# Optimization experiments

Measured on AMD Instinct MI355X. Metric: run time of the kernel, lower is better.

## Reference

```python
import jax, jax.numpy as jnp
import numpy as np

NC = 128      # nc
K = 5         # cube kernel size
NS = 3        # n_scale pyramid levels
NV = 150000   # vertices (cortical-surface scale)
NF = 300000   # faces ~ 2*NV
L = 192       # volume side (L = W = H -> rescale = [1,1,1])


def setup_inputs() -> dict:
    key = jax.random.key(0)
    ks = jax.random.split(key, 16)
    s = 0.05
    return {
        "v": jax.random.uniform(ks[0], (1, NV, 3), minval=-0.9, maxval=0.9, dtype=jnp.float32),
        "f": jax.random.randint(ks[1], (1, NF, 3), 0, NV, dtype=jnp.int32),
        "volume": jax.random.normal(ks[2], (1, 1, L, L, L), dtype=jnp.float32),
        "fc1_w": jax.random.normal(ks[3], (6, NC), dtype=jnp.float32) * s,
        "fc1_b": jnp.zeros((NC,), jnp.float32),
        "fc2_w": jax.random.normal(ks[4], (2 * NC, 4 * NC), dtype=jnp.float32) * s,
        "fc2_b": jnp.zeros((4 * NC,), jnp.float32),
        "fc3_w": jax.random.normal(ks[5], (4 * NC, 2 * NC), dtype=jnp.float32) * s,
        "fc3_b": jnp.zeros((2 * NC,), jnp.float32),
        "fc4_w": jax.random.normal(ks[6], (2 * NC, 3), dtype=jnp.float32) * s,
        "fc4_b": jnp.zeros((3,), jnp.float32),
        "conv_w": jax.random.normal(ks[7], (NC, NS, K, K, K), dtype=jnp.float32) * s,
        "conv_b": jnp.zeros((NC,), jnp.float32),
        "lfc_w": jax.random.normal(ks[8], (NC, NC), dtype=jnp.float32) * s,
        "lfc_b": jnp.zeros((NC,), jnp.float32),
    }


def _vertex_normals(v, f):
    # pytorch3d-style vertex normals: scatter-add area-weighted face normals, then normalize.
    verts, faces = v[0], f[0]
    p0, p1, p2 = verts[faces[:, 0]], verts[faces[:, 1]], verts[faces[:, 2]]
    fn = jnp.cross(p1 - p0, p2 - p0)  # [NF, 3]
    n = jnp.zeros_like(verts)
    n = n.at[faces[:, 0]].add(fn).at[faces[:, 1]].add(fn).at[faces[:, 2]].add(fn)
    n = n / jnp.maximum(jnp.linalg.norm(n, axis=-1, keepdims=True), 1e-12)
    return n[None]  # [1, NV, 3]


def _cube_sampling(v, volume):
    # Vectorized version of the 125-iteration Python gather loop:
    # gather a KxKxK neighborhood per vertex at each pyramid scale.
    vol_n = volume[0, 0]
    off = jnp.arange(-(K - 1) // 2, (K - 1) // 2 + 1)  # [-2..2]
    cubes = []
    for n in range(NS):
        if n > 0:
            s = vol_n.shape[0]
            vol_n = vol_n.reshape(s // 2, 2, s // 2, 2, s // 2, 2).mean(axis=(1, 3, 5))  # avg_pool3d(2)
        idx = jnp.round((v[0] + 1.0) * L / 2 ** (n + 1)).astype(jnp.int32)  # rescale = [1,1,1]
        idx = jnp.clip(idx, (K - 1) // 2, L // 2 ** n - 3)
        i0 = idx[:, 0, None, None, None] + off[None, :, None, None]
        i1 = idx[:, 1, None, None, None] + off[None, None, :, None]
        i2 = idx[:, 2, None, None, None] + off[None, None, None, :]
        cubes.append(vol_n[i0, i1, i2])  # [NV, K, K, K]
    return jnp.stack(cubes, axis=1)  # [NV, NS, K, K, K]


def reference(v, f, volume, fc1_w, fc1_b, fc2_w, fc2_b, fc3_w, fc3_b, fc4_w, fc4_b,
              conv_w, conv_b, lfc_w, lfc_b):
    coord = v
    normal = _vertex_normals(v, f)
    x = jnp.concatenate([v, normal], axis=2)                 # [1, NV, 6]
    x = jax.nn.leaky_relu(x @ fc1_w + fc1_b, 0.15)           # [1, NV, NC]
    cubes = _cube_sampling(v, volume)                        # [NV, NS, K, K, K]
    # Conv3d with kernel == input size -> single output voxel == full contraction.
    x_local = jnp.einsum('ncijk,ocijk->no', cubes, conv_w) + conv_b  # [NV, NC]
    x_local = (x_local @ lfc_w + lfc_b)[None]                # [1, NV, NC]
    x = jnp.concatenate([x, x_local], axis=2)                # [1, NV, 2*NC]
    x = jax.nn.leaky_relu(x @ fc2_w + fc2_b, 0.15)
    x = jax.nn.leaky_relu(x @ fc3_w + fc3_b, 0.15)
    x = jnp.tanh(x @ fc4_w + fc4_b) * 0.1
    return coord + x
```

## Files before the change

### kernel.cpp

```cpp
#include <hip/hip_runtime.h>
#include <hip/hip_bf16.h>
#include <math.h>

#define NVERT 150000
#define NFACE 300000
#define LVOL  192
#define TVB   32
#define MTV   48

#define NB_NORM   1172
#define NB_POOL1  3456
#define NB_POOL2  432
#define NB_PW     1024
#define NB_PC     193
#define NB_CP0    3456
#define POOL1_START (NB_NORM)
#define POOL2_START (NB_NORM + NB_POOL1)
#define PW_START    (NB_NORM + NB_POOL1 + NB_POOL2)
#define PC_START    (NB_NORM + NB_POOL1 + NB_POOL2 + NB_PW)
#define NB_MEGA     (NB_NORM + NB_POOL1 + NB_POOL2 + NB_PW + NB_PC)

#define WS_BIG_NEED 44808576ull
#define WS_B16_NEED 58964352ull

typedef short v8s __attribute__((ext_vector_type(8)));
typedef float v4f __attribute__((ext_vector_type(4)));

__device__ __forceinline__ float s2f(short s) {
    unsigned int u = ((unsigned int)(unsigned short)s) << 16;
    return __builtin_bit_cast(float, u);
}
__device__ __forceinline__ short f2s(float f) {
    __hip_bfloat16 h = __float2bfloat16(f);
    return __builtin_bit_cast(short, h);
}
__device__ __forceinline__ float lrelu(float x) { return x > 0.f ? x : 0.15f * x; }

__device__ __forceinline__ float ldf(const void* __restrict__ p, int i, int bf) {
    return bf ? s2f(((const short*)p)[i]) : ((const float*)p)[i];
}

__device__ __forceinline__ int haddr(int r, int c) {
    int hi  = c >> 7;
    int mid = (c >> 4) & 7;
    int lo  = c & 15;
    int wc  = hi * 64 + (mid & 3) * 16 + lo;
    return ((mid < 4) ? 0 : 12672) + r * 264 + wc;
}

__global__ void detect_kernel(const void* __restrict__ v, int* __restrict__ flag) {
    __shared__ int s_ok;
    int t = threadIdx.x;
    if (t == 0) s_ok = 1;
    __syncthreads();
    float x = s2f(((const short*)v)[t]);
    if (!(fabsf(x) <= 1.0f)) atomicAnd(&s_ok, 0);
    __syncthreads();
    if (t == 0) *flag = s_ok;
}

__global__ __launch_bounds__(256) void mega_prep_kernel(
    const void* __restrict__ v, const int* __restrict__ f, float* __restrict__ n_accum,
    const void* __restrict__ volume,
    short* __restrict__ vol1b, short* __restrict__ vol2b,
    const void* __restrict__ fc2_w, const void* __restrict__ fc3_w,
    short* __restrict__ fc2T, short* __restrict__ fc3T,
    const void* __restrict__ conv_w, const void* __restrict__ lfc_w,
    const void* __restrict__ conv_b, const void* __restrict__ lfc_b,
    short* __restrict__ Wcomb, float* __restrict__ bcomb,
    const int* __restrict__ flag,
    short* __restrict__ vol0b)
{
    const int bf = *flag;
    const int bid = blockIdx.x;
    const int t = threadIdx.x;

    if (bid < NB_NORM) {
        int ft = bid * 256 + t;
        if (ft >= NFACE) return;
        int i0 = f[ft * 3 + 0], i1 = f[ft * 3 + 1], i2 = f[ft * 3 + 2];
        float p0x = ldf(v, i0 * 3 + 0, bf), p0y = ldf(v, i0 * 3 + 1, bf), p0z = ldf(v, i0 * 3 + 2, bf);
        float p1x = ldf(v, i1 * 3 + 0, bf), p1y = ldf(v, i1 * 3 + 1, bf), p1z = ldf(v, i1 * 3 + 2, bf);
        float p2x = ldf(v, i2 * 3 + 0, bf), p2y = ldf(v, i2 * 3 + 1, bf), p2z = ldf(v, i2 * 3 + 2, bf);
        float e1x = p1x - p0x, e1y = p1y - p0y, e1z = p1z - p0z;
        float e2x = p2x - p0x, e2y = p2y - p0y, e2z = p2z - p0z;
        float cx = e1y * e2z - e1z * e2y;
        float cy = e1z * e2x - e1x * e2z;
        float cz = e1x * e2y - e1y * e2x;
        atomicAdd(&n_accum[i0 * 3 + 0], cx); atomicAdd(&n_accum[i0 * 3 + 1], cy); atomicAdd(&n_accum[i0 * 3 + 2], cz);
        atomicAdd(&n_accum[i1 * 3 + 0], cx); atomicAdd(&n_accum[i1 * 3 + 1], cy); atomicAdd(&n_accum[i1 * 3 + 2], cz);
        atomicAdd(&n_accum[i2 * 3 + 0], cx); atomicAdd(&n_accum[i2 * 3 + 1], cy); atomicAdd(&n_accum[i2 * 3 + 2], cz);
    } else if (bid < POOL2_START) {
        int id = (bid - POOL1_START) * 256 + t;
        int z = id % 96, y = (id / 96) % 96, x = id / (96 * 96);
        float s = 0.f;
        #pragma unroll
        for (int a = 0; a < 2; a++)
            #pragma unroll
            for (int b = 0; b < 2; b++)
                #pragma unroll
                for (int c = 0; c < 2; c++)
                    s += ldf(volume, (2 * x + a) * (LVOL * LVOL) + (2 * y + b) * LVOL + (2 * z + c), bf);
        s *= 0.125f;
        vol1b[id] = f2s(s);
    } else if (bid < PW_START) {
        int id = (bid - POOL2_START) * 256 + t;
        int z = id % 48, y = (id / 48) % 48, x = id / (48 * 48);
        float s = 0.f;
        for (int a = 0; a < 4; a++)
            for (int b = 0; b < 4; b++)
                #pragma unroll
                for (int c = 0; c < 4; c++)
                    s += ldf(volume, (4 * x + a) * (LVOL * LVOL) + (4 * y + b) * LVOL + (4 * z + c), bf);
        s *= 0.015625f;
        vol2b[id] = f2s(s);
    } else if (bid < PC_START) {
        int id = (bid - PW_START) * 256 + t;
        if (id < 131072) {
            int col = id >> 8, k = id & 255;
            int tile = col >> 4, ln = col & 15;
            int kk = k >> 5, r = k & 31, qq = r >> 3, e = r & 7;
            fc2T[((tile * 8 + kk) * 64 + qq * 16 + ln) * 8 + e] = f2s(ldf(fc2_w, k * 512 + col, bf));
        } else {
            int i = id - 131072;
            int col = i >> 9, k = i & 511;
            int tile = col >> 4, ln = col & 15;
            int kk = k >> 5, r = k & 31, qq = r >> 3, e = r & 7;
            fc3T[((tile * 16 + kk) * 64 + qq * 16 + ln) * 8 + e] = f2s(ldf(fc3_w, k * 256 + col, bf));
        }
    } else if (bid < NB_MEGA) {
        int id = (bid - PC_START) * 256 + t;
        if (id < 49152) {
            int j = id / 384, k = id - j * 384;
            float acc = 0.f;
            if (k < 375) {
                float a0 = 0.f, a1 = 0.f, a2 = 0.f, a3 = 0.f;
                for (int o = 0; o < 128; o += 4) {
                    a0 += ldf(conv_w, (o + 0) * 375 + k, bf) * ldf(lfc_w, (o + 0) * 128 + j, bf);
                    a1 += ldf(conv_w, (o + 1) * 375 + k, bf) * ldf(lfc_w, (o + 1) * 128 + j, bf);
                    a2 += ldf(conv_w, (o + 2) * 375 + k, bf) * ldf(lfc_w, (o + 2) * 128 + j, bf);
                    a3 += ldf(conv_w, (o + 3) * 375 + k, bf) * ldf(lfc_w, (o + 3) * 128 + j, bf);
                }
                acc = (a0 + a1) + (a2 + a3);
            }
            int tile = j >> 4, ln = j & 15;
            int kk = k >> 5, r = k & 31, qq = r >> 3, e = r & 7;
            Wcomb[((tile * 12 + kk) * 64 + qq * 16 + ln) * 8 + e] = f2s(acc);
        } else if (id < 49152 + 128) {
            int j = id - 49152;
            float acc = ldf(lfc_b, j, bf);
            for (int o = 0; o < 128; o++) acc += ldf(conv_b, o, bf) * ldf(lfc_w, o * 128 + j, bf);
            bcomb[j] = acc;
        }
    } else {
        if (bf) return;
        int id = (bid - NB_MEGA) * 2048 + t * 8;
        const float* vp = (const float*)volume;
        short tmp[8];
        #pragma unroll
        for (int i = 0; i < 8; i++) tmp[i] = f2s(vp[id + i]);
        *(v8s*)&vol0b[id] = *(v8s*)tmp;
    }
}


__global__ __launch_bounds__(256, 6) void gather_conv_kernel(
    const void* __restrict__ v,
    const void* __restrict__ volume,
    const short* __restrict__ vol1b,
    const short* __restrict__ vol2b,
    const short* __restrict__ vol0b,
    const short* __restrict__ Wcomb,
    const float* __restrict__ bcomb,
    short* __restrict__ xloc,
    const int* __restrict__ flag)
{
    __shared__ __align__(16) short sCube[TVB * 392];
    __shared__ int sIdx[TVB * 4];

    const int bf = *flag;
    const int t = threadIdx.x;
    const int base = blockIdx.x * TVB;
    const int w = t >> 6, L = t & 63, q = L >> 4, ln = L & 15;
    const short* v0 = bf ? (const short*)volume : vol0b;

    if (t < TVB) {
        int vert = min(base + t, NVERT - 1);
        float vx = ldf(v, vert * 3 + 0, bf);
        float vy = ldf(v, vert * 3 + 1, bf);
        float vz = ldf(v, vert * 3 + 2, bf);
        #pragma unroll
        for (int n = 0; n < 3; n++) {
            float scl = (n == 0) ? 96.0f : (n == 1 ? 48.0f : 24.0f);
            int dim = LVOL >> n, lim = dim - 3;
            int cx = min(max((int)rintf((vx + 1.0f) * scl), 2), lim);
            int cy = min(max((int)rintf((vy + 1.0f) * scl), 2), lim);
            int cz = min(max((int)rintf((vz + 1.0f) * scl), 2), lim);
            sIdx[t * 4 + n] = (cx * dim + cy) * dim + (cz - 2);
        }
    }
    __syncthreads();

    for (int idx = t; idx < TVB * 75; idx += 256) {
        int n   = idx / 800;
        int rem = idx - n * 800;
        int vl  = rem / 25;
        int dd  = rem - vl * 25;
        int di  = dd / 5, dj = dd - di * 5;
        int dim = LVOL >> n;
        int addr = sIdx[vl * 4 + n] + (di - 2) * dim * dim + (dj - 2) * dim;
        short* dst = &sCube[vl * 392 + n * 125 + dd * 5];
        if (n == 0 && v0 == nullptr) {
            const float* vp = (const float*)volume;
            #pragma unroll
            for (int i = 0; i < 5; i++) dst[i] = f2s(vp[addr + i]);
        } else {
            const short* lvl = (n == 0) ? v0 : (n == 1 ? vol1b : vol2b);
            #pragma unroll
            for (int i = 0; i < 5; i++) dst[i] = lvl[addr + i];
        }
    }
    for (int idx = t; idx < TVB * 9; idx += 256) {
        int vl = idx / 9, rr = idx - vl * 9;
        sCube[vl * 392 + 375 + rr] = 0;
    }
    __syncthreads();

    #pragma unroll
    for (int nt = 0; nt < 2; nt++) {
        int col = w * 32 + nt * 16 + ln;
        const short* wb = Wcomb + ((w * 2 + nt) * 12 * 64 + q * 16 + ln) * 8;
        v4f acc0 = {0.f, 0.f, 0.f, 0.f}, acc1 = {0.f, 0.f, 0.f, 0.f};
        #pragma unroll
        for (int k0 = 0; k0 < 12; k0++) {
            v8s b  = *(const v8s*)(wb + k0 * 512);
            v8s a0 = *(const v8s*)&sCube[ln * 392 + k0 * 32 + q * 8];
            v8s a1 = *(const v8s*)&sCube[(16 + ln) * 392 + k0 * 32 + q * 8];
            acc0 = __builtin_amdgcn_mfma_f32_16x16x32_bf16(a0, b, acc0, 0, 0, 0);
            acc1 = __builtin_amdgcn_mfma_f32_16x16x32_bf16(a1, b, acc1, 0, 0, 0);
        }
        float bias = bcomb[col];
        #pragma unroll
        for (int r = 0; r < 4; r++) {
            xloc[(base + q * 4 + r) * 128 + col]      = f2s(acc0[r] + bias);
            xloc[(base + 16 + q * 4 + r) * 128 + col] = f2s(acc1[r] + bias);
        }
    }
}

__global__ __launch_bounds__(256, 3) void mlp_kernel(
    const void* __restrict__ v,
    const float* __restrict__ n_accum,
    const short* __restrict__ xloc,
    const short* __restrict__ fc2T,
    const short* __restrict__ fc3T,
    const void* __restrict__ fc1_w, const void* __restrict__ fc1_b,
    const void* __restrict__ fc2_b, const void* __restrict__ fc3_b,
    const void* __restrict__ fc4_w, const void* __restrict__ fc4_b,
    void* __restrict__ out,
    const int* __restrict__ flag)
{
    __shared__ __align__(16) char smem[52224];
    short* sX  = (short*)smem;
    short* sHB = (short*)smem;
    short* s3  = (short*)smem;
    short* sW4 = (short*)(smem + 50688);

    const int bf = *flag;
    const int t = threadIdx.x;
    const int base = blockIdx.x * MTV;
    const int w = t >> 6, L = t & 63, q = L >> 4, ln = L & 15;
    const int laneoff = (q * 16 + ln) * 8;

    for (int id = t; id < MTV * 16; id += 256) {
        int row = id >> 4, seg = id & 15;
        v8s x = *(const v8s*)(xloc + (base + row) * 128 + seg * 8);
        *(v8s*)&sX[row * 264 + 128 + seg * 8] = x;
    }

    for (int i = t; i < 768; i += 256) {
        int j = i >> 8, k = i & 255;
        sW4[i] = f2s(ldf(fc4_w, k * 3 + j, bf));
    }

    {
        int vi = t >> 2, cb = (t & 3) * 32;
        if (vi < MTV) {
            int vert = base + vi;
            float i0 = ldf(v, vert * 3 + 0, bf);
            float i1 = ldf(v, vert * 3 + 1, bf);
            float i2 = ldf(v, vert * 3 + 2, bf);
            float nx = n_accum[vert * 3 + 0];
            float ny = n_accum[vert * 3 + 1];
            float nz = n_accum[vert * 3 + 2];
            float inv = 1.0f / fmaxf(sqrtf(nx * nx + ny * ny + nz * nz), 1e-12f);
            float i3 = nx * inv, i4 = ny * inv, i5 = nz * inv;
            #pragma unroll 8
            for (int i = 0; i < 32; i++) {
                int c = cb + i;
                float acc = ldf(fc1_b, c, bf)
                          + i0 * ldf(fc1_w, 0 * 128 + c, bf)
                          + i1 * ldf(fc1_w, 1 * 128 + c, bf)
                          + i2 * ldf(fc1_w, 2 * 128 + c, bf)
                          + i3 * ldf(fc1_w, 3 * 128 + c, bf)
                          + i4 * ldf(fc1_w, 4 * 128 + c, bf)
                          + i5 * ldf(fc1_w, 5 * 128 + c, bf);
                sX[vi * 264 + c] = f2s(lrelu(acc));
            }
        }
    }
    __syncthreads();

    {
        #pragma unroll
        for (int nt = 4; nt < 8; nt++) {
            int col = w * 128 + nt * 16 + ln;
            const short* bb = fc2T + (w * 8 + nt) * 8 * 512 + laneoff;
            v4f acc0 = {0.f, 0.f, 0.f, 0.f}, acc1 = {0.f, 0.f, 0.f, 0.f}, acc2 = {0.f, 0.f, 0.f, 0.f};
            #pragma unroll
            for (int k0 = 0; k0 < 8; k0++) {
                v8s b  = *(const v8s*)(bb + k0 * 512);
                v8s a0 = *(const v8s*)&sX[(ln) * 264 + k0 * 32 + q * 8];
                v8s a1 = *(const v8s*)&sX[(16 + ln) * 264 + k0 * 32 + q * 8];
                v8s a2 = *(const v8s*)&sX[(32 + ln) * 264 + k0 * 32 + q * 8];
                acc0 = __builtin_amdgcn_mfma_f32_16x16x32_bf16(a0, b, acc0, 0, 0, 0);
                acc1 = __builtin_amdgcn_mfma_f32_16x16x32_bf16(a1, b, acc1, 0, 0, 0);
                acc2 = __builtin_amdgcn_mfma_f32_16x16x32_bf16(a2, b, acc2, 0, 0, 0);
            }
            float bias = ldf(fc2_b, col, bf);
            int wc = 12672 + w * 64 + (nt - 4) * 16 + ln;
            #pragma unroll
            for (int r = 0; r < 4; r++) {
                sHB[(q * 4 + r) * 264 + wc]      = f2s(lrelu(acc0[r] + bias));
                sHB[(16 + q * 4 + r) * 264 + wc] = f2s(lrelu(acc1[r] + bias));
                sHB[(32 + q * 4 + r) * 264 + wc] = f2s(lrelu(acc2[r] + bias));
            }
        }

        v4f accL[4][3];
        #pragma unroll
        for (int nt = 0; nt < 4; nt++)
            #pragma unroll
            for (int m = 0; m < 3; m++)
                accL[nt][m] = (v4f){0.f, 0.f, 0.f, 0.f};

        #pragma unroll
        for (int nt = 0; nt < 4; nt++) {
            const short* bb = fc2T + (w * 8 + nt) * 8 * 512 + laneoff;
            #pragma unroll
            for (int k0 = 0; k0 < 8; k0++) {
                v8s b  = *(const v8s*)(bb + k0 * 512);
                v8s a0 = *(const v8s*)&sX[(ln) * 264 + k0 * 32 + q * 8];
                v8s a1 = *(const v8s*)&sX[(16 + ln) * 264 + k0 * 32 + q * 8];
                v8s a2 = *(const v8s*)&sX[(32 + ln) * 264 + k0 * 32 + q * 8];
                accL[nt][0] = __builtin_amdgcn_mfma_f32_16x16x32_bf16(a0, b, accL[nt][0], 0, 0, 0);
                accL[nt][1] = __builtin_amdgcn_mfma_f32_16x16x32_bf16(a1, b, accL[nt][1], 0, 0, 0);
                accL[nt][2] = __builtin_amdgcn_mfma_f32_16x16x32_bf16(a2, b, accL[nt][2], 0, 0, 0);
            }
        }
        __syncthreads();

        #pragma unroll
        for (int nt = 0; nt < 4; nt++) {
            int col = w * 128 + nt * 16 + ln;
            float bias = ldf(fc2_b, col, bf);
            int wc = w * 64 + nt * 16 + ln;
            #pragma unroll
            for (int r = 0; r < 4; r++) {
                sHB[(q * 4 + r) * 264 + wc]      = f2s(lrelu(accL[nt][0][r] + bias));
                sHB[(16 + q * 4 + r) * 264 + wc] = f2s(lrelu(accL[nt][1][r] + bias));
                sHB[(32 + q * 4 + r) * 264 + wc] = f2s(lrelu(accL[nt][2][r] + bias));
            }
        }
    }
    __syncthreads();

    {
        v4f acc[4][3];
        #pragma unroll
        for (int nt = 0; nt < 4; nt++)
            #pragma unroll
            for (int m = 0; m < 3; m++)
                acc[nt][m] = (v4f){0.f, 0.f, 0.f, 0.f};

        #pragma unroll
        for (int half = 0; half < 2; half++) {
            v8s A0[8], A1[8], A2[8];
            #pragma unroll
            for (int k0 = 0; k0 < 8; k0++) {
                int c = half * 256 + k0 * 32 + q * 8;
                A0[k0] = *(const v8s*)&sHB[haddr(ln, c)];
                A1[k0] = *(const v8s*)&sHB[haddr(16 + ln, c)];
                A2[k0] = *(const v8s*)&sHB[haddr(32 + ln, c)];
            }
            #pragma unroll
            for (int nt = 0; nt < 4; nt++) {
                const short* bb = fc3T + ((w * 4 + nt) * 16 + half * 8) * 512 + laneoff;
                v8s B[8];
                #pragma unroll
                for (int k0 = 0; k0 < 8; k0++) B[k0] = *(const v8s*)(bb + k0 * 512);
                #pragma unroll
                for (int k0 = 0; k0 < 8; k0++) {
                    acc[nt][0] = __builtin_amdgcn_mfma_f32_16x16x32_bf16(A0[k0], B[k0], acc[nt][0], 0, 0, 0);
                    acc[nt][1] = __builtin_amdgcn_mfma_f32_16x16x32_bf16(A1[k0], B[k0], acc[nt][1], 0, 0, 0);
                    acc[nt][2] = __builtin_amdgcn_mfma_f32_16x16x32_bf16(A2[k0], B[k0], acc[nt][2], 0, 0, 0);
                }
            }
        }
        __syncthreads();

        #pragma unroll
        for (int nt = 0; nt < 4; nt++) {
            int col = w * 64 + nt * 16 + ln;
            float bias = ldf(fc3_b, col, bf);
            #pragma unroll
            for (int r = 0; r < 4; r++) {
                s3[(q * 4 + r) * 264 + col]      = f2s(lrelu(acc[nt][0][r] + bias));
                s3[(16 + q * 4 + r) * 264 + col] = f2s(lrelu(acc[nt][1][r] + bias));
                s3[(32 + q * 4 + r) * 264 + col] = f2s(lrelu(acc[nt][2][r] + bias));
            }
        }
    }
    __syncthreads();

    {
        int vi = t >> 2, l = t & 3;
        if (vi < MTV) {
            float p0 = 0.f, p1 = 0.f, p2 = 0.f;
            for (int k = l * 8; k < 256; k += 32) {
                #pragma unroll
                for (int j = 0; j < 8; j++) {
                    float a = s2f(s3[vi * 264 + k + j]);
                    p0 += a * s2f(sW4[0 * 256 + k + j]);
                    p1 += a * s2f(sW4[1 * 256 + k + j]);
                    p2 += a * s2f(sW4[2 * 256 + k + j]);
                }
            }
            #pragma unroll
            for (int s = 2; s; s >>= 1) {
                p0 += __shfl_down(p0, s, 4);
                p1 += __shfl_down(p1, s, 4);
                p2 += __shfl_down(p2, s, 4);
            }
            if (l == 0) {
                int vert = base + vi;
                float vx = ldf(v, vert * 3 + 0, bf);
                float vy = ldf(v, vert * 3 + 1, bf);
                float vz = ldf(v, vert * 3 + 2, bf);
                float o0 = vx + 0.1f * tanhf(p0 + ldf(fc4_b, 0, bf));
                float o1 = vy + 0.1f * tanhf(p1 + ldf(fc4_b, 1, bf));
                float o2 = vz + 0.1f * tanhf(p2 + ldf(fc4_b, 2, bf));
                if (bf) {
                    short* ob = (short*)out;
                    ob[vert * 3 + 0] = f2s(o0);
                    ob[vert * 3 + 1] = f2s(o1);
                    ob[vert * 3 + 2] = f2s(o2);
                } else {
                    float* of = (float*)out;
                    of[vert * 3 + 0] = o0;
                    of[vert * 3 + 1] = o1;
                    of[vert * 3 + 2] = o2;
                }
            }
        }
    }
}

__global__ __launch_bounds__(256, 3) void fused_mfma_kernel(
    const void* __restrict__ v,
    const float* __restrict__ n_accum,
    const void* __restrict__ volume,
    const short* __restrict__ vol1,
    const short* __restrict__ vol2,
    const short* __restrict__ Wcomb,
    const float* __restrict__ bcomb,
    const short* __restrict__ fc2T,
    const short* __restrict__ fc3T,
    const void* __restrict__ fc1_w, const void* __restrict__ fc1_b,
    const void* __restrict__ fc2_b, const void* __restrict__ fc3_b,
    const void* __restrict__ fc4_w, const void* __restrict__ fc4_b,
    void* __restrict__ out,
    const int* __restrict__ flag)
{
    __shared__ __align__(16) char smem[51712];
    short* sX    = (short*)smem;
    short* sCube = (short*)(smem + 16896);
    short* sH    = (short*)(smem + 16896);
    short* s3    = (short*)smem;
    short* sW4   = (short*)(smem + 50176);

    const int bf = *flag;
    const int t = threadIdx.x;
    const int base = blockIdx.x * TVB;
    const int w = t >> 6, L = t & 63, q = L >> 4, ln = L & 15;
    const int laneoff = (q * 16 + ln) * 8;

    for (int idx = t; idx < TVB * 75; idx += 256) {
        int vl  = idx / 75;
        int r75 = idx - vl * 75;
        int n   = r75 / 25;
        int dd  = r75 - n * 25;
        int di  = dd / 5, dj = dd - di * 5;
        int vert = base + vl;
        short* dst = &sCube[vl * 392 + n * 125 + dd * 5];
        if (vert < NVERT) {
            float vx = ldf(v, vert * 3 + 0, bf);
            float vy = ldf(v, vert * 3 + 1, bf);
            float vz = ldf(v, vert * 3 + 2, bf);
            float scl = (n == 0) ? 96.0f : (n == 1 ? 48.0f : 24.0f);
            int lim = (LVOL >> n) - 3;
            int cx = (int)rintf((vx + 1.0f) * scl);
            int cy = (int)rintf((vy + 1.0f) * scl);
            int cz = (int)rintf((vz + 1.0f) * scl);
            cx = min(max(cx, 2), lim) + di - 2;
            cy = min(max(cy, 2), lim) + dj - 2;
            cz = min(max(cz, 2), lim);
            if (n == 0) {
                int b0 = (cx * LVOL + cy) * LVOL + (cz - 2);
                if (bf) {
                    const short* vp = (const short*)volume;
                    #pragma unroll
                    for (int i = 0; i < 5; i++) dst[i] = vp[b0 + i];
                } else {
                    const float* vp = (const float*)volume;
                    #pragma unroll
                    for (int i = 0; i < 5; i++) dst[i] = f2s(vp[b0 + i]);
                }
            } else {
                const short* lvl = (n == 1) ? vol1 : vol2;
                int dim = (n == 1) ? 96 : 48;
                int b0 = (cx * dim + cy) * dim + (cz - 2);
                #pragma unroll
                for (int i = 0; i < 5; i++) dst[i] = lvl[b0 + i];
            }
        } else {
            #pragma unroll
            for (int i = 0; i < 5; i++) dst[i] = 0;
        }
    }
    for (int idx = t; idx < TVB * 9; idx += 256) {
        int vl = idx / 9, rr = idx - vl * 9;
        sCube[vl * 392 + 375 + rr] = 0;
    }
    for (int i = t; i < 768; i += 256) {
        int j = i >> 8, k = i & 255;
        sW4[i] = f2s(ldf(fc4_w, k * 3 + j, bf));
    }
    {
        int vi = t & 31, cb = (t >> 5) * 16;
        int vert = base + vi;
        float i0 = 0.f, i1 = 0.f, i2 = 0.f, i3 = 0.f, i4 = 0.f, i5 = 0.f;
        if (vert < NVERT) {
            i0 = ldf(v, vert * 3 + 0, bf);
            i1 = ldf(v, vert * 3 + 1, bf);
            i2 = ldf(v, vert * 3 + 2, bf);
            float nx = n_accum[vert * 3 + 0];
            float ny = n_accum[vert * 3 + 1];
            float nz = n_accum[vert * 3 + 2];
            float inv = 1.0f / fmaxf(sqrtf(nx * nx + ny * ny + nz * nz), 1e-12f);
            i3 = nx * inv; i4 = ny * inv; i5 = nz * inv;
        }
        #pragma unroll
        for (int i = 0; i < 16; i++) {
            int c = cb + i;
            float acc = ldf(fc1_b, c, bf)
                      + i0 * ldf(fc1_w, 0 * 128 + c, bf)
                      + i1 * ldf(fc1_w, 1 * 128 + c, bf)
                      + i2 * ldf(fc1_w, 2 * 128 + c, bf)
                      + i3 * ldf(fc1_w, 3 * 128 + c, bf)
                      + i4 * ldf(fc1_w, 4 * 128 + c, bf)
                      + i5 * ldf(fc1_w, 5 * 128 + c, bf);
            sX[vi * 264 + c] = f2s(lrelu(acc));
        }
    }
    __syncthreads();

    #pragma unroll
    for (int nt = 0; nt < 2; nt++) {
        int col = w * 32 + nt * 16 + ln;
        const short* wb = Wcomb + ((w * 2 + nt) * 12 * 64) * 8 + laneoff;
        v4f acc0 = {0.f, 0.f, 0.f, 0.f}, acc1 = {0.f, 0.f, 0.f, 0.f};
        #pragma unroll
        for (int k0 = 0; k0 < 12; k0++) {
            v8s b  = *(const v8s*)(wb + k0 * 512);
            v8s a0 = *(const v8s*)&sCube[ln * 392 + k0 * 32 + q * 8];
            v8s a1 = *(const v8s*)&sCube[(16 + ln) * 392 + k0 * 32 + q * 8];
            acc0 = __builtin_amdgcn_mfma_f32_16x16x32_bf16(a0, b, acc0, 0, 0, 0);
            acc1 = __builtin_amdgcn_mfma_f32_16x16x32_bf16(a1, b, acc1, 0, 0, 0);
        }
        float bias = bcomb[col];
        #pragma unroll
        for (int r = 0; r < 4; r++) {
            sX[(q * 4 + r) * 264 + 128 + col]      = f2s(acc0[r] + bias);
            sX[(16 + q * 4 + r) * 264 + 128 + col] = f2s(acc1[r] + bias);
        }
    }
    __syncthreads();

    {
        v8s a0[8], a1[8];
        #pragma unroll
        for (int k0 = 0; k0 < 8; k0++) {
            a0[k0] = *(const v8s*)&sX[ln * 264 + k0 * 32 + q * 8];
            a1[k0] = *(const v8s*)&sX[(16 + ln) * 264 + k0 * 32 + q * 8];
        }
        #pragma unroll
        for (int nt = 0; nt < 8; nt++) {
            int col = w * 128 + nt * 16 + ln;
            const short* bb = fc2T + (w * 8 + nt) * 8 * 512 + laneoff;
            v4f acc0 = {0.f, 0.f, 0.f, 0.f}, acc1 = {0.f, 0.f, 0.f, 0.f};
            #pragma unroll
            for (int k0 = 0; k0 < 8; k0++) {
                v8s b = *(const v8s*)(bb + k0 * 512);
                acc0 = __builtin_amdgcn_mfma_f32_16x16x32_bf16(a0[k0], b, acc0, 0, 0, 0);
                acc1 = __builtin_amdgcn_mfma_f32_16x16x32_bf16(a1[k0], b, acc1, 0, 0, 0);
            }
            float bias = ldf(fc2_b, col, bf);
            #pragma unroll
            for (int r = 0; r < 4; r++) {
                sH[(q * 4 + r) * 520 + col]      = f2s(lrelu(acc0[r] + bias));
                sH[(16 + q * 4 + r) * 520 + col] = f2s(lrelu(acc1[r] + bias));
            }
        }
    }
    __syncthreads();

    {
        #pragma unroll
        for (int nt = 0; nt < 4; nt++) {
            int col = w * 64 + nt * 16 + ln;
            v4f acc0 = {0.f, 0.f, 0.f, 0.f}, acc1 = {0.f, 0.f, 0.f, 0.f};
            #pragma unroll
            for (int half = 0; half < 2; half++) {
                const short* bb = fc3T + ((w * 4 + nt) * 16 + half * 8) * 512 + laneoff;
                #pragma unroll
                for (int k0 = 0; k0 < 8; k0++) {
                    v8s b  = *(const v8s*)(bb + k0 * 512);
                    v8s a0 = *(const v8s*)&sH[ln * 520 + half * 256 + k0 * 32 + q * 8];
                    v8s a1 = *(const v8s*)&sH[(16 + ln) * 520 + half * 256 + k0 * 32 + q * 8];
                    acc0 = __builtin_amdgcn_mfma_f32_16x16x32_bf16(a0, b, acc0, 0, 0, 0);
                    acc1 = __builtin_amdgcn_mfma_f32_16x16x32_bf16(a1, b, acc1, 0, 0, 0);
                }
            }
            float bias = ldf(fc3_b, col, bf);
            #pragma unroll
            for (int r = 0; r < 4; r++) {
                s3[(q * 4 + r) * 264 + col]      = f2s(lrelu(acc0[r] + bias));
                s3[(16 + q * 4 + r) * 264 + col] = f2s(lrelu(acc1[r] + bias));
            }
        }
    }
    __syncthreads();

    {
        int vi = t >> 3, l = t & 7;
        float p0 = 0.f, p1 = 0.f, p2 = 0.f;
        for (int k = l; k < 256; k += 8) {
            float a = s2f(s3[vi * 264 + k]);
            p0 += a * s2f(sW4[0 * 256 + k]);
            p1 += a * s2f(sW4[1 * 256 + k]);
            p2 += a * s2f(sW4[2 * 256 + k]);
        }
        #pragma unroll
        for (int s = 4; s; s >>= 1) {
            p0 += __shfl_down(p0, s, 8);
            p1 += __shfl_down(p1, s, 8);
            p2 += __shfl_down(p2, s, 8);
        }
        if (l == 0) {
            int vert = base + vi;
            if (vert < NVERT) {
                float vx = ldf(v, vert * 3 + 0, bf);
                float vy = ldf(v, vert * 3 + 1, bf);
                float vz = ldf(v, vert * 3 + 2, bf);
                float o0 = vx + 0.1f * tanhf(p0 + ldf(fc4_b, 0, bf));
                float o1 = vy + 0.1f * tanhf(p1 + ldf(fc4_b, 1, bf));
                float o2 = vz + 0.1f * tanhf(p2 + ldf(fc4_b, 2, bf));
                if (bf) {
                    short* ob = (short*)out;
                    ob[vert * 3 + 0] = f2s(o0);
                    ob[vert * 3 + 1] = f2s(o1);
                    ob[vert * 3 + 2] = f2s(o2);
                } else {
                    float* of = (float*)out;
                    of[vert * 3 + 0] = o0;
                    of[vert * 3 + 1] = o1;
                    of[vert * 3 + 2] = o2;
                }
            }
        }
    }
}

extern "C" void kernel_launch(void* const* d_in, const int* in_sizes, int n_in,
                              void* d_out, int out_size, void* d_ws, size_t ws_size,
                              hipStream_t stream) {
    const void* v      = d_in[0];
    const int*  f      = (const int*)d_in[1];
    const void* volume = d_in[2];
    const void* fc1_w  = d_in[3];
    const void* fc1_b  = d_in[4];
    const void* fc2_w  = d_in[5];
    const void* fc2_b  = d_in[6];
    const void* fc3_w  = d_in[7];
    const void* fc3_b  = d_in[8];
    const void* fc4_w  = d_in[9];
    const void* fc4_b  = d_in[10];
    const void* conv_w = d_in[11];
    const void* conv_b = d_in[12];
    const void* lfc_w  = d_in[13];
    const void* lfc_b  = d_in[14];

    char* wsb = (char*)d_ws;
    const int big = (ws_size >= WS_BIG_NEED) ? 1 : 0;
    const int b16 = (ws_size >= WS_B16_NEED) ? 1 : 0;

    if (big) {
        int*   flag    = (int*)wsb;
        float* n_accum = (float*)(wsb + 64);
        short* vol1b   = (short*)(wsb + 1800064);
        short* vol2b   = (short*)(wsb + 5339008);
        short* Wcomb   = (short*)(wsb + 5781376);
        float* bcomb   = (float*)(wsb + 5879680);
        short* fc2T    = (short*)(wsb + 5880192);
        short* fc3T    = (short*)(wsb + 6142336);
        short* xloc    = (short*)(wsb + 6404480);
        short* vol0b   = b16 ? (short*)(wsb + 44808576) : nullptr;

        hipMemsetAsync(n_accum, 0, NVERT * 3 * sizeof(float), stream);
        detect_kernel<<<1, 256, 0, stream>>>(v, flag);
        mega_prep_kernel<<<NB_MEGA + (b16 ? NB_CP0 : 0), 256, 0, stream>>>(
            v, f, n_accum, volume,
            vol1b, vol2b,
            fc2_w, fc3_w, fc2T, fc3T,
            conv_w, lfc_w, conv_b, lfc_b, Wcomb, bcomb, flag, vol0b);
        gather_conv_kernel<<<(NVERT + TVB - 1) / TVB, 256, 0, stream>>>(
            v, volume, vol1b, vol2b, vol0b, Wcomb, bcomb, xloc, flag);
        mlp_kernel<<<(NVERT + MTV - 1) / MTV, 256, 0, stream>>>(
            v, n_accum, xloc, fc2T, fc3T,
            fc1_w, fc1_b, fc2_b, fc3_b, fc4_w, fc4_b, d_out, flag);
    } else {
        int*   flag    = (int*)wsb;
        float* n_accum = (float*)(wsb + 64);
        short* vol1    = (short*)(wsb + 1800064);
        short* vol2    = (short*)(wsb + 3569536);
        short* Wcomb   = (short*)(wsb + 3790720);
        float* bcomb   = (float*)(wsb + 3889024);
        short* fc2T    = (short*)(wsb + 3889536);
        short* fc3T    = (short*)(wsb + 4151680);

        hipMemsetAsync(n_accum, 0, NVERT * 3 * sizeof(float), stream);
        detect_kernel<<<1, 256, 0, stream>>>(v, flag);
        mega_prep_kernel<<<NB_MEGA, 256, 0, stream>>>(
            v, f, n_accum, volume,
            vol1, vol2,
            fc2_w, fc3_w, fc2T, fc3T,
            conv_w, lfc_w, conv_b, lfc_b, Wcomb, bcomb, flag, nullptr);
        fused_mfma_kernel<<<(NVERT + TVB - 1) / TVB, 256, 0, stream>>>(
            v, n_accum, volume, vol1, vol2, Wcomb, bcomb, fc2T, fc3T,
            fc1_w, fc1_b, fc2_b, fc3_b, fc4_w, fc4_b, d_out, flag);
    }
}
```

Measured before the change: 536.6 us.

## Move normal scatter and weight transposes into gather kernel's extra blocks

The face-normal atomic scatter and the fc2/fc3 weight transpose-to-bf16 work move out of the prep kernel and into trailing blocks of the gather/conv kernel. The prep kernel now holds only the pooling, combined-weight and volume-cast work that the gather depends on. The normal and transpose work can then overlap with the gather, which does not need their outputs. In exchange, the small-workspace path gains an extra kernel launch, and the added branch may change the register budget of the gather kernel.

Measured after the change: 534.0 us. No clear change (-0.5%).

```diff
diff --git a/kernel.cpp b/kernel.cpp
--- a/kernel.cpp
+++ b/kernel.cpp
@@ -8,17 +8,16 @@
 #define TVB   32
 #define MTV   48
 
-#define NB_NORM   1172
-#define NB_POOL1  3456
-#define NB_POOL2  432
-#define NB_PW     1024
-#define NB_PC     193
-#define NB_CP0    3456
-#define POOL1_START (NB_NORM)
-#define POOL2_START (NB_NORM + NB_POOL1)
-#define PW_START    (NB_NORM + NB_POOL1 + NB_POOL2)
-#define PC_START    (NB_NORM + NB_POOL1 + NB_POOL2 + NB_PW)
-#define NB_MEGA     (NB_NORM + NB_POOL1 + NB_POOL2 + NB_PW + NB_PC)
+#define P2_POOL1 3456
+#define P2_POOL2 432
+#define P2_WC    193
+#define P2_CP0   3456
+#define P2_POOL2_START (P2_POOL1)
+#define P2_WC_START    (P2_POOL1 + P2_POOL2)
+#define P2_CP0_START   (P2_POOL1 + P2_POOL2 + P2_WC)
+
+#define NB_NORM 1172
+#define NB_TRS  1024
 
 #define WS_BIG_NEED 44808576ull
 #define WS_B16_NEED 58964352ull
@@ -59,12 +58,9 @@
     if (t == 0) *flag = s_ok;
 }
 
-__global__ __launch_bounds__(256) void mega_prep_kernel(
-    const void* __restrict__ v, const int* __restrict__ f, float* __restrict__ n_accum,
+__global__ __launch_bounds__(256) void mega_prep2_kernel(
     const void* __restrict__ volume,
     short* __restrict__ vol1b, short* __restrict__ vol2b,
-    const void* __restrict__ fc2_w, const void* __restrict__ fc3_w,
-    short* __restrict__ fc2T, short* __restrict__ fc3T,
     const void* __restrict__ conv_w, const void* __restrict__ lfc_w,
     const void* __restrict__ conv_b, const void* __restrict__ lfc_b,
     short* __restrict__ Wcomb, float* __restrict__ bcomb,
@@ -75,23 +71,8 @@
     const int bid = blockIdx.x;
     const int t = threadIdx.x;
 
-    if (bid < NB_NORM) {
-        int ft = bid * 256 + t;
-        if (ft >= NFACE) return;
-        int i0 = f[ft * 3 + 0], i1 = f[ft * 3 + 1], i2 = f[ft * 3 + 2];
-        float p0x = ldf(v, i0 * 3 + 0, bf), p0y = ldf(v, i0 * 3 + 1, bf), p0z = ldf(v, i0 * 3 + 2, bf);
-        float p1x = ldf(v, i1 * 3 + 0, bf), p1y = ldf(v, i1 * 3 + 1, bf), p1z = ldf(v, i1 * 3 + 2, bf);
-        float p2x = ldf(v, i2 * 3 + 0, bf), p2y = ldf(v, i2 * 3 + 1, bf), p2z = ldf(v, i2 * 3 + 2, bf);
-        float e1x = p1x - p0x, e1y = p1y - p0y, e1z = p1z - p0z;
-        float e2x = p2x - p0x, e2y = p2y - p0y, e2z = p2z - p0z;
-        float cx = e1y * e2z - e1z * e2y;
-        float cy = e1z * e2x - e1x * e2z;
-        float cz = e1x * e2y - e1y * e2x;
-        atomicAdd(&n_accum[i0 * 3 + 0], cx); atomicAdd(&n_accum[i0 * 3 + 1], cy); atomicAdd(&n_accum[i0 * 3 + 2], cz);
-        atomicAdd(&n_accum[i1 * 3 + 0], cx); atomicAdd(&n_accum[i1 * 3 + 1], cy); atomicAdd(&n_accum[i1 * 3 + 2], cz);
-        atomicAdd(&n_accum[i2 * 3 + 0], cx); atomicAdd(&n_accum[i2 * 3 + 1], cy); atomicAdd(&n_accum[i2 * 3 + 2], cz);
-    } else if (bid < POOL2_START) {
-        int id = (bid - POOL1_START) * 256 + t;
+    if (bid < P2_POOL1) {
+        int id = bid * 256 + t;
         int z = id % 96, y = (id / 96) % 96, x = id / (96 * 96);
         float s = 0.f;
         #pragma unroll
@@ -103,8 +84,8 @@
                     s += ldf(volume, (2 * x + a) * (LVOL * LVOL) + (2 * y + b) * LVOL + (2 * z + c), bf);
         s *= 0.125f;
         vol1b[id] = f2s(s);
-    } else if (bid < PW_START) {
-        int id = (bid - POOL2_START) * 256 + t;
+    } else if (bid < P2_WC_START) {
+        int id = (bid - P2_POOL2_START) * 256 + t;
         int z = id % 48, y = (id / 48) % 48, x = id / (48 * 48);
         float s = 0.f;
         for (int a = 0; a < 4; a++)
@@ -114,22 +95,8 @@
                     s += ldf(volume, (4 * x + a) * (LVOL * LVOL) + (4 * y + b) * LVOL + (4 * z + c), bf);
         s *= 0.015625f;
         vol2b[id] = f2s(s);
-    } else if (bid < PC_START) {
-        int id = (bid - PW_START) * 256 + t;
-        if (id < 131072) {
-            int col = id >> 8, k = id & 255;
-            int tile = col >> 4, ln = col & 15;
-            int kk = k >> 5, r = k & 31, qq = r >> 3, e = r & 7;
-            fc2T[((tile * 8 + kk) * 64 + qq * 16 + ln) * 8 + e] = f2s(ldf(fc2_w, k * 512 + col, bf));
-        } else {
-            int i = id - 131072;
-            int col = i >> 9, k = i & 511;
-            int tile = col >> 4, ln = col & 15;
-            int kk = k >> 5, r = k & 31, qq = r >> 3, e = r & 7;
-            fc3T[((tile * 16 + kk) * 64 + qq * 16 + ln) * 8 + e] = f2s(ldf(fc3_w, k * 256 + col, bf));
-        }
-    } else if (bid < NB_MEGA) {
-        int id = (bid - PC_START) * 256 + t;
+    } else if (bid < P2_CP0_START) {
+        int id = (bid - P2_WC_START) * 256 + t;
         if (id < 49152) {
             int j = id / 384, k = id - j * 384;
             float acc = 0.f;
@@ -154,7 +121,7 @@
         }
     } else {
         if (bf) return;
-        int id = (bid - NB_MEGA) * 2048 + t * 8;
+        int id = (bid - P2_CP0_START) * 2048 + t * 8;
         const float* vp = (const float*)volume;
         short tmp[8];
         #pragma unroll
@@ -163,24 +130,63 @@
     }
 }
 
-
-__global__ __launch_bounds__(256, 6) void gather_conv_kernel(
+__global__ __launch_bounds__(256, 6) void gather_ext_kernel(
     const void* __restrict__ v,
+    const int* __restrict__ f, float* __restrict__ n_accum,
     const void* __restrict__ volume,
     const short* __restrict__ vol1b,
     const short* __restrict__ vol2b,
     const short* __restrict__ vol0b,
     const short* __restrict__ Wcomb,
     const float* __restrict__ bcomb,
+    const void* __restrict__ fc2_w, const void* __restrict__ fc3_w,
+    short* __restrict__ fc2T, short* __restrict__ fc3T,
     short* __restrict__ xloc,
-    const int* __restrict__ flag)
+    const int* __restrict__ flag, int ngather)
 {
     __shared__ __align__(16) short sCube[TVB * 392];
     __shared__ int sIdx[TVB * 4];
 
     const int bf = *flag;
     const int t = threadIdx.x;
-    const int base = blockIdx.x * TVB;
+    const int bid = blockIdx.x;
+
+    if (bid >= ngather) {
+        int rb = bid - ngather;
+        if (rb < NB_NORM) {
+            int ft = rb * 256 + t;
+            if (ft >= NFACE) return;
+            int i0 = f[ft * 3 + 0], i1 = f[ft * 3 + 1], i2 = f[ft * 3 + 2];
+            float p0x = ldf(v, i0 * 3 + 0, bf), p0y = ldf(v, i0 * 3 + 1, bf), p0z = ldf(v, i0 * 3 + 2, bf);
+            float p1x = ldf(v, i1 * 3 + 0, bf), p1y = ldf(v, i1 * 3 + 1, bf), p1z = ldf(v, i1 * 3 + 2, bf);
+            float p2x = ldf(v, i2 * 3 + 0, bf), p2y = ldf(v, i2 * 3 + 1, bf), p2z = ldf(v, i2 * 3 + 2, bf);
+            float e1x = p1x - p0x, e1y = p1y - p0y, e1z = p1z - p0z;
+            float e2x = p2x - p0x, e2y = p2y - p0y, e2z = p2z - p0z;
+            float cx = e1y * e2z - e1z * e2y;
+            float cy = e1z * e2x - e1x * e2z;
+            float cz = e1x * e2y - e1y * e2x;
+            atomicAdd(&n_accum[i0 * 3 + 0], cx); atomicAdd(&n_accum[i0 * 3 + 1], cy); atomicAdd(&n_accum[i0 * 3 + 2], cz);
+            atomicAdd(&n_accum[i1 * 3 + 0], cx); atomicAdd(&n_accum[i1 * 3 + 1], cy); atomicAdd(&n_accum[i1 * 3 + 2], cz);
+            atomicAdd(&n_accum[i2 * 3 + 0], cx); atomicAdd(&n_accum[i2 * 3 + 1], cy); atomicAdd(&n_accum[i2 * 3 + 2], cz);
+        } else {
+            int id = (rb - NB_NORM) * 256 + t;
+            if (id < 131072) {
+                int col = id >> 8, k = id & 255;
+                int tile = col >> 4, ln = col & 15;
+                int kk = k >> 5, r = k & 31, qq = r >> 3, e = r & 7;
+                fc2T[((tile * 8 + kk) * 64 + qq * 16 + ln) * 8 + e] = f2s(ldf(fc2_w, k * 512 + col, bf));
+            } else {
+                int i = id - 131072;
+                int col = i >> 9, k = i & 511;
+                int tile = col >> 4, ln = col & 15;
+                int kk = k >> 5, r = k & 31, qq = r >> 3, e = r & 7;
+                fc3T[((tile * 16 + kk) * 64 + qq * 16 + ln) * 8 + e] = f2s(ldf(fc3_w, k * 256 + col, bf));
+            }
+        }
+        return;
+    }
+
+    const int base = bid * TVB;
     const int w = t >> 6, L = t & 63, q = L >> 4, ln = L & 15;
     const short* v0 = bf ? (const short*)volume : vol0b;
 
@@ -729,13 +735,13 @@
 
         hipMemsetAsync(n_accum, 0, NVERT * 3 * sizeof(float), stream);
         detect_kernel<<<1, 256, 0, stream>>>(v, flag);
-        mega_prep_kernel<<<NB_MEGA + (b16 ? NB_CP0 : 0), 256, 0, stream>>>(
-            v, f, n_accum, volume,
-            vol1b, vol2b,
-            fc2_w, fc3_w, fc2T, fc3T,
+        mega_prep2_kernel<<<P2_CP0_START + (b16 ? P2_CP0 : 0), 256, 0, stream>>>(
+            volume, vol1b, vol2b,
             conv_w, lfc_w, conv_b, lfc_b, Wcomb, bcomb, flag, vol0b);
-        gather_conv_kernel<<<(NVERT + TVB - 1) / TVB, 256, 0, stream>>>(
-            v, volume, vol1b, vol2b, vol0b, Wcomb, bcomb, xloc, flag);
+        int ngather = (NVERT + TVB - 1) / TVB;
+        gather_ext_kernel<<<ngather + NB_NORM + NB_TRS, 256, 0, stream>>>(
+            v, f, n_accum, volume, vol1b, vol2b, vol0b, Wcomb, bcomb,
+            fc2_w, fc3_w, fc2T, fc3T, xloc, flag, ngather);
         mlp_kernel<<<(NVERT + MTV - 1) / MTV, 256, 0, stream>>>(
             v, n_accum, xloc, fc2T, fc3T,
             fc1_w, fc1_b, fc2_b, fc3_b, fc4_w, fc4_b, d_out, flag);
@@ -751,11 +757,12 @@
 
         hipMemsetAsync(n_accum, 0, NVERT * 3 * sizeof(float), stream);
         detect_kernel<<<1, 256, 0, stream>>>(v, flag);
-        mega_prep_kernel<<<NB_MEGA, 256, 0, stream>>>(
-            v, f, n_accum, volume,
-            vol1, vol2,
-            fc2_w, fc3_w, fc2T, fc3T,
+        mega_prep2_kernel<<<P2_CP0_START, 256, 0, stream>>>(
+            volume, vol1, vol2,
             conv_w, lfc_w, conv_b, lfc_b, Wcomb, bcomb, flag, nullptr);
+        gather_ext_kernel<<<NB_NORM + NB_TRS, 256, 0, stream>>>(
+            v, f, n_accum, volume, vol1, vol2, nullptr, Wcomb, bcomb,
+            fc2_w, fc3_w, fc2T, fc3T, nullptr, flag, 0);
         fused_mfma_kernel<<<(NVERT + TVB - 1) / TVB, 256, 0, stream>>>(
             v, n_accum, volume, vol1, vol2, Wcomb, bcomb, fc2T, fc3T,
             fc1_w, fc1_b, fc2_b, fc3_b, fc4_w, fc4_b, d_out, flag);
```
